# Kernel optimization log

Hardware: AMD Instinct MI355X
Metric: run time of the kernel (lower is better)

## Reference

```python
import jax, jax.numpy as jnp
import numpy as np

H = W = 1024
CHUNK = 32  # rows per chunk in the column EDT pass (keeps intermediate at 32*H*W floats)


def setup_inputs() -> dict:
    key = jax.random.key(0)
    k1, k2 = jax.random.split(key)
    preds = jax.random.randint(k1, (H, W), 0, 2).astype(jnp.float32)
    targets = jax.random.randint(k2, (H, W), 0, 2).astype(jnp.float32)
    return {"preds": preds, "targets": targets}


def _edges(seg):
    # morphological erosion via 3x3 box conv, threshold at 9 == kernel.numel()
    s = seg[None, None]  # (1,1,H,W)
    kern = jnp.ones((1, 1, 3, 3), seg.dtype)
    conv = jax.lax.conv_general_dilated(s, kern, (1, 1), ((1, 1), (1, 1)))
    eroded = (conv[0, 0] == 9.0).astype(seg.dtype)
    return seg - eroded


def _edt(edges):
    # exact Euclidean distance transform: distance to nearest zero of (1 - edges),
    # i.e. nearest pixel where edges == 1.  Separable exact algorithm:
    #   1) per-row 1D distance to nearest feature (via cummax/cummin scans)
    #   2) per-column lower envelope min_k g2[k,j] + (i-k)^2 (chunked brute force)
    feat = (1.0 - edges) == 0.0
    Hh, Ww = edges.shape
    BIG = jnp.float32(1e6)
    col = jnp.arange(Ww, dtype=jnp.float32)
    left = col - jax.lax.cummax(jnp.where(feat, col, -BIG), axis=1)
    right = jax.lax.cummin(jnp.where(feat, col, BIG), axis=1, reverse=True) - col
    g = jnp.minimum(jnp.minimum(left, right), BIG)  # row-wise 1D distance
    g2 = g * g  # (H,W) squared row distances
    rows = jnp.arange(Hh, dtype=jnp.float32)

    def chunk(ic):  # ic: (CHUNK,) target row indices
        # (CHUNK, H, W): g2[k,j] + (i-k)^2, min over source row k
        d = g2[None, :, :] + (ic[:, None, None] - rows[None, :, None]) ** 2
        return jnp.min(d, axis=1)  # (CHUNK, W)

    D2 = jax.lax.map(chunk, rows.reshape(-1, CHUNK)).reshape(Hh, Ww)
    return jnp.sqrt(D2)


def reference(preds, targets):
    pred_edges = _edges(preds)
    target_edges = _edges(targets)
    # scipy EDT ran on detached CPU copies -> no gradient through the DTs
    pred_dt = jax.lax.stop_gradient(_edt(pred_edges))
    target_dt = jax.lax.stop_gradient(_edt(target_edges))
    pred_err = target_edges * pred_dt
    target_err = pred_edges * target_dt
    loss = (jnp.mean(pred_err) + jnp.mean(target_err)) / 2.0
    return jax.nn.sigmoid(loss)
```

## Files before the change

### kernel.cpp

```cpp
#include <hip/hip_runtime.h>
#include <math.h>


#define HW 1024
#define WIN 8
#define RPB 128
#define KROWS (RPB + 2 * WIN)
#define HS_STRIDE 17
#define NC 146
#define NW 130
#define NBYTES ((NC + NW) * 16)

__device__ inline int edge_at(const float* __restrict__ seg, int k, int j)
{
    if ((unsigned)k >= (unsigned)HW || (unsigned)j >= (unsigned)HW) return 0;
    if (seg[k * HW + j] == 0.f) return 0;
    bool all9 = true;
    #pragma unroll
    for (int dy = -1; dy <= 1; ++dy)
        #pragma unroll
        for (int dx = -1; dx <= 1; ++dx) {
            const int kk = k + dy, jj = j + dx;
            const float v = ((unsigned)kk < (unsigned)HW && (unsigned)jj < (unsigned)HW)
                            ? seg[kk * HW + jj] : 0.f;
            all9 = all9 && (v != 0.f);
        }
    return all9 ? 0 : 1;
}

__global__ __launch_bounds__(256)
void k_main(const float* __restrict__ pred, const float* __restrict__ targ,
            float* __restrict__ partial)
{
    const int t  = threadIdx.x;
    const int j0 = blockIdx.x * 16;
    const int i0 = blockIdx.y * RPB;
    const int mc = blockIdx.z;
    const float* __restrict__ segc = mc ? targ : pred;
    const float* __restrict__ segw = mc ? pred : targ;

    __shared__ alignas(16) unsigned char sbytes[NBYTES];
    __shared__ unsigned long long s_mc[NC];
    __shared__ unsigned long long s_me[NW];
    __shared__ float hs[KROWS * HS_STRIDE];
    __shared__ unsigned short esb[RPB];
    __shared__ float wsum[4];

    const int W0 = j0 - 24;

    for (int idx = t; idx < NBYTES; idx += 256) {
        const int  isW = idx >= NC * 16;
        const int  rel = isW ? idx - NC * 16 : idx;
        const int  row = rel >> 4, c4 = rel & 15;
        const int  gr  = isW ? (i0 - 1 + row) : (i0 - 9 + row);
        const int  c   = W0 + c4 * 4;
        float4 v = make_float4(0.f, 0.f, 0.f, 0.f);
        if ((unsigned)gr < (unsigned)HW && (unsigned)c <= 1020u) {
            const float* __restrict__ base = isW ? segw : segc;
            v = *(const float4*)&base[gr * HW + c];
        }
        const unsigned by = (unsigned)(v.x != 0.f) | ((unsigned)(v.y != 0.f) << 1)
                          | ((unsigned)(v.z != 0.f) << 2) | ((unsigned)(v.w != 0.f) << 3);
        sbytes[idx] = (unsigned char)by;
    }
    __syncthreads();

    for (int rowi = t; rowi < NC + NW; rowi += 256) {
        const uint4 u = *(const uint4*)&sbytes[rowi * 16];
        const unsigned wq[4] = {u.x, u.y, u.z, u.w};
        unsigned long long r = 0ull;
        #pragma unroll
        for (int q = 0; q < 4; ++q) {
            const unsigned x = wq[q] & 0x0F0F0F0Fu;
            const unsigned y = x | (x >> 4);
            const unsigned h16 = (y & 0xFFu) | (((y >> 16) & 0xFFu) << 8);
            r |= (unsigned long long)h16 << (16 * q);
        }
        if (rowi < NC) s_mc[rowi] = r;
        else           s_me[rowi - NC] = r;
    }
    __syncthreads();

    if (t < KROWS) {
        const int kr = i0 - WIN + t;
        if ((unsigned)kr < (unsigned)HW) {
            const unsigned long long sA = s_mc[t], sB = s_mc[t + 1], sC = s_mc[t + 2];
            const unsigned long long va = sA & sB & sC;
            const unsigned long long er = va & (va << 1) & (va >> 1);
            const unsigned long long edge = (sB & ~er) & 0x7FFFFFFFFFFFFFFEull;
            const float krk = (float)(kr * kr);
            #pragma unroll
            for (int jc = 0; jc < 16; ++jc) {
                const int p = 24 + jc;
                const unsigned long long mle = edge & ((1ull << (p + 1)) - 1ull);
                const unsigned long long mge = edge >> p;
                int g = 1 << 20;
                if (mle) g = p - (63 - __clzll((long long)mle));
                if (mge) g = min(g, __ffsll((unsigned long long)mge) - 1);
                hs[t * HS_STRIDE + jc] = (g < (1 << 20))
                    ? fmaf((float)g, (float)g, krk) : 1e30f;
            }
        } else {
            #pragma unroll
            for (int jc = 0; jc < 16; ++jc)
                hs[t * HS_STRIDE + jc] = 1e30f;
        }
    }
    if (t < RPB) {
        const unsigned long long sA = s_me[t], sB = s_me[t + 1], sC = s_me[t + 2];
        const unsigned long long va = sA & sB & sC;
        const unsigned long long er = va & (va << 1) & (va >> 1);
        const unsigned long long edge = sB & ~er;
        esb[t] = (unsigned short)((edge >> 24) & 0xFFFFull);
    }
    __syncthreads();

    const int jj = t & 15;
    const int iw = t >> 4;
    float lsum = 0.f;

    #pragma unroll
    for (int g = 0; g < 2; ++g) {
        const int ib = i0 + iw * 8 + g * 4;
        const int kkS = iw * 8 + g * 4;
        float b0 = 3e38f, b1 = 3e38f, b2 = 3e38f, b3 = 3e38f;
        float kf = (float)(ib - WIN);
        const float m0 = -2.f * (float)(ib);
        const float m1 = -2.f * (float)(ib + 1);
        const float m2 = -2.f * (float)(ib + 2);
        const float m3 = -2.f * (float)(ib + 3);
        #pragma unroll
        for (int kk = kkS; kk < kkS + 2 * WIN + 4; ++kk) {
            const float hvv = hs[kk * HS_STRIDE + jj];
            b0 = fminf(b0, fmaf(m0, kf, hvv));
            b1 = fminf(b1, fmaf(m1, kf, hvv));
            b2 = fminf(b2, fmaf(m2, kf, hvv));
            b3 = fminf(b3, fmaf(m3, kf, hvv));
            kf += 1.f;
        }
        const int sLo = max(0, ib - WIN);
        const int sHi = min(HW - 1, ib + WIN + 3);
        float bs[4] = {b0, b1, b2, b3};
        #pragma unroll
        for (int w = 0; w < 4; ++w) {
            const int i = ib + w;
            float D2 = (float)(i * i) + bs[w];
            const int dl = i - sLo + 1, dr = sHi + 1 - i;
            const bool need = (D2 > 576.f) ||
                              ((sLo > 0) && (D2 > (float)(dl * dl))) ||
                              ((sHi < HW - 1) && (D2 > (float)(dr * dr)));
            if (need) {
                const int jg = j0 + jj;
                float bb = 1e6f - (float)jg;
                bb = bb * bb;
                for (int k = 0; k < HW; ++k) {
                    const float rowt = (float)((i - k) * (i - k));
                    if (rowt >= bb) continue;
                    for (int d = 0; d < HW; ++d) {
                        const float dd = rowt + (float)(d * d);
                        if (dd >= bb) break;
                        if (edge_at(segc, k, jg - d) || edge_at(segc, k, jg + d)) {
                            bb = dd; break;
                        }
                    }
                }
                D2 = bb;
            }
            const unsigned wbit = (esb[i - i0] >> jj) & 1u;
            lsum += wbit ? sqrtf(D2) : 0.f;
        }
    }

    #pragma unroll
    for (int off = 32; off > 0; off >>= 1) lsum += __shfl_down(lsum, off);
    if ((t & 63) == 0) wsum[t >> 6] = lsum;
    __syncthreads();
    if (t == 0) {
        const int bid = blockIdx.x + 64 * (blockIdx.y + 8 * blockIdx.z);
        partial[bid] = wsum[0] + wsum[1] + wsum[2] + wsum[3];
    }
}

__global__ __launch_bounds__(256)
void k_fin(const float* __restrict__ partial, float* __restrict__ out)
{
    const int t = threadIdx.x;
    float s = partial[t] + partial[t + 256] + partial[t + 512] + partial[t + 768];
    #pragma unroll
    for (int off = 32; off > 0; off >>= 1) s += __shfl_down(s, off);
    __shared__ float w[4];
    if ((t & 63) == 0) w[t >> 6] = s;
    __syncthreads();
    if (t == 0) {
        const float tot = w[0] + w[1] + w[2] + w[3];
        const float loss = tot * (1.f / (2.f * 1024.f * 1024.f));
        out[0] = 1.f / (1.f + expf(-loss));
    }
}

extern "C" void kernel_launch(void* const* d_in, const int* in_sizes, int n_in,
                              void* d_out, int out_size, void* d_ws, size_t ws_size,
                              hipStream_t stream)
{
    const float* preds   = (const float*)d_in[0];
    const float* targets = (const float*)d_in[1];
    float* out = (float*)d_out;

    float* partial = (float*)d_ws;

    dim3 gM(HW / 16, HW / RPB, 2);
    k_main<<<gM, 256, 0, stream>>>(preds, targets, partial);

    k_fin<<<1, 256, 0, stream>>>(partial, out);
}
```

Measured before the change: 79.26 us.

## Process both images per block with wider 32-column tiles and shared loads

Each block now loads both pred and target for one tile, builds bitmasks for both once, and runs the windowed EDT for each image in turn. The tile widens from 16 to 32 columns, which narrows the halo to 16 and lowers the fallback threshold from 576 to 256. The grid drops from 1024 to 256 blocks, so there is less redundant halo loading but fewer blocks and more serial work per block. The lower threshold may send more pixels down the slow brute-force fallback path.

```diff
diff --git a/kernel.cpp b/kernel.cpp
--- a/kernel.cpp
+++ b/kernel.cpp
@@ -6,10 +6,9 @@
 #define WIN 8
 #define RPB 128
 #define KROWS (RPB + 2 * WIN)
-#define HS_STRIDE 17
-#define NC 146
-#define NW 130
-#define NBYTES ((NC + NW) * 16)
+#define HS_STRIDE 33
+#define NR 146
+#define NBY (2 * NR * 16)
 
 __device__ inline int edge_at(const float* __restrict__ seg, int k, int j)
 {
@@ -28,101 +27,50 @@
     return all9 ? 0 : 1;
 }
 
-__global__ __launch_bounds__(256)
-void k_main(const float* __restrict__ pred, const float* __restrict__ targ,
-            float* __restrict__ partial)
-{
-    const int t  = threadIdx.x;
-    const int j0 = blockIdx.x * 16;
-    const int i0 = blockIdx.y * RPB;
-    const int mc = blockIdx.z;
-    const float* __restrict__ segc = mc ? targ : pred;
-    const float* __restrict__ segw = mc ? pred : targ;
-
-    __shared__ alignas(16) unsigned char sbytes[NBYTES];
-    __shared__ unsigned long long s_mc[NC];
-    __shared__ unsigned long long s_me[NW];
-    __shared__ float hs[KROWS * HS_STRIDE];
-    __shared__ unsigned short esb[RPB];
-    __shared__ float wsum[4];
-
-    const int W0 = j0 - 24;
-
-    for (int idx = t; idx < NBYTES; idx += 256) {
-        const int  isW = idx >= NC * 16;
-        const int  rel = isW ? idx - NC * 16 : idx;
-        const int  row = rel >> 4, c4 = rel & 15;
-        const int  gr  = isW ? (i0 - 1 + row) : (i0 - 9 + row);
-        const int  c   = W0 + c4 * 4;
-        float4 v = make_float4(0.f, 0.f, 0.f, 0.f);
-        if ((unsigned)gr < (unsigned)HW && (unsigned)c <= 1020u) {
-            const float* __restrict__ base = isW ? segw : segc;
-            v = *(const float4*)&base[gr * HW + c];
-        }
-        const unsigned by = (unsigned)(v.x != 0.f) | ((unsigned)(v.y != 0.f) << 1)
-                          | ((unsigned)(v.z != 0.f) << 2) | ((unsigned)(v.w != 0.f) << 3);
-        sbytes[idx] = (unsigned char)by;
-    }
-    __syncthreads();
-
-    for (int rowi = t; rowi < NC + NW; rowi += 256) {
-        const uint4 u = *(const uint4*)&sbytes[rowi * 16];
-        const unsigned wq[4] = {u.x, u.y, u.z, u.w};
-        unsigned long long r = 0ull;
-        #pragma unroll
-        for (int q = 0; q < 4; ++q) {
-            const unsigned x = wq[q] & 0x0F0F0F0Fu;
-            const unsigned y = x | (x >> 4);
-            const unsigned h16 = (y & 0xFFu) | (((y >> 16) & 0xFFu) << 8);
-            r |= (unsigned long long)h16 << (16 * q);
-        }
-        if (rowi < NC) s_mc[rowi] = r;
-        else           s_me[rowi - NC] = r;
-    }
-    __syncthreads();
-
-    if (t < KROWS) {
-        const int kr = i0 - WIN + t;
+__device__ __forceinline__ void fill_hs(float* __restrict__ hs,
+                                        const unsigned long long* __restrict__ mm,
+                                        int i0, int t)
+{
+    for (int idx = t; idx < 288; idx += 256) {
+        const int tt = idx >> 1, half = idx & 1;
+        const int kr = i0 - WIN + tt;
+        float* __restrict__ hrow = &hs[tt * HS_STRIDE + half * 16];
         if ((unsigned)kr < (unsigned)HW) {
-            const unsigned long long sA = s_mc[t], sB = s_mc[t + 1], sC = s_mc[t + 2];
+            const unsigned long long sA = mm[tt], sB = mm[tt + 1], sC = mm[tt + 2];
             const unsigned long long va = sA & sB & sC;
             const unsigned long long er = va & (va << 1) & (va >> 1);
             const unsigned long long edge = (sB & ~er) & 0x7FFFFFFFFFFFFFFEull;
             const float krk = (float)(kr * kr);
             #pragma unroll
             for (int jc = 0; jc < 16; ++jc) {
-                const int p = 24 + jc;
+                const int p = 16 + half * 16 + jc;
                 const unsigned long long mle = edge & ((1ull << (p + 1)) - 1ull);
                 const unsigned long long mge = edge >> p;
                 int g = 1 << 20;
                 if (mle) g = p - (63 - __clzll((long long)mle));
-                if (mge) g = min(g, __ffsll((unsigned long long)mge) - 1);
-                hs[t * HS_STRIDE + jc] = (g < (1 << 20))
-                    ? fmaf((float)g, (float)g, krk) : 1e30f;
+                if (mge) g = min(g, __ffsll(mge) - 1);
+                hrow[jc] = (g < (1 << 20)) ? fmaf((float)g, (float)g, krk) : 1e30f;
             }
         } else {
             #pragma unroll
-            for (int jc = 0; jc < 16; ++jc)
-                hs[t * HS_STRIDE + jc] = 1e30f;
-        }
-    }
-    if (t < RPB) {
-        const unsigned long long sA = s_me[t], sB = s_me[t + 1], sC = s_me[t + 2];
-        const unsigned long long va = sA & sB & sC;
-        const unsigned long long er = va & (va << 1) & (va >> 1);
-        const unsigned long long edge = sB & ~er;
-        esb[t] = (unsigned short)((edge >> 24) & 0xFFFFull);
-    }
-    __syncthreads();
-
-    const int jj = t & 15;
-    const int iw = t >> 4;
+            for (int jc = 0; jc < 16; ++jc) hrow[jc] = 1e30f;
+        }
+    }
+}
+
+__device__ __forceinline__ float edt_acc(const float* __restrict__ hs,
+                                         const unsigned* __restrict__ esbw,
+                                         int i0, int j0, int t,
+                                         const float* __restrict__ segf)
+{
+    const int jj = t & 31;
+    const int iw = t >> 5;
     float lsum = 0.f;
 
     #pragma unroll
-    for (int g = 0; g < 2; ++g) {
-        const int ib = i0 + iw * 8 + g * 4;
-        const int kkS = iw * 8 + g * 4;
+    for (int g = 0; g < 4; ++g) {
+        const int ib = i0 + iw * 16 + g * 4;
+        const int kkS = iw * 16 + g * 4;
         float b0 = 3e38f, b1 = 3e38f, b2 = 3e38f, b3 = 3e38f;
         float kf = (float)(ib - WIN);
         const float m0 = -2.f * (float)(ib);
@@ -146,7 +94,7 @@
             const int i = ib + w;
             float D2 = (float)(i * i) + bs[w];
             const int dl = i - sLo + 1, dr = sHi + 1 - i;
-            const bool need = (D2 > 576.f) ||
+            const bool need = (D2 > 256.f) ||
                               ((sLo > 0) && (D2 > (float)(dl * dl))) ||
                               ((sHi < HW - 1) && (D2 > (float)(dr * dr)));
             if (need) {
@@ -159,24 +107,93 @@
                     for (int d = 0; d < HW; ++d) {
                         const float dd = rowt + (float)(d * d);
                         if (dd >= bb) break;
-                        if (edge_at(segc, k, jg - d) || edge_at(segc, k, jg + d)) {
+                        if (edge_at(segf, k, jg - d) || edge_at(segf, k, jg + d)) {
                             bb = dd; break;
                         }
                     }
                 }
                 D2 = bb;
             }
-            const unsigned wbit = (esb[i - i0] >> jj) & 1u;
+            const unsigned wbit = (esbw[i - i0] >> jj) & 1u;
             lsum += wbit ? sqrtf(D2) : 0.f;
         }
     }
+    return lsum;
+}
+
+__global__ __launch_bounds__(256)
+void k_main(const float* __restrict__ pred, const float* __restrict__ targ,
+            float* __restrict__ partial)
+{
+    const int t  = threadIdx.x;
+    const int j0 = blockIdx.x * 32;
+    const int i0 = blockIdx.y * RPB;
+
+    __shared__ alignas(16) unsigned char sbytes[NBY];
+    __shared__ unsigned long long s_m[2 * NR];
+    __shared__ float hs[KROWS * HS_STRIDE];
+    __shared__ unsigned esb[2][RPB];
+    __shared__ float wsum[4];
+
+    const int W0 = j0 - 16;
+
+    for (int idx = t; idx < NBY; idx += 256) {
+        const int  img = idx >= NR * 16;
+        const int  rel = img ? idx - NR * 16 : idx;
+        const int  row = rel >> 4, c4 = rel & 15;
+        const int  gr  = i0 - 9 + row;
+        const int  c   = W0 + c4 * 4;
+        float4 v = make_float4(0.f, 0.f, 0.f, 0.f);
+        if ((unsigned)gr < (unsigned)HW && (unsigned)c <= 1020u) {
+            const float* __restrict__ base = img ? targ : pred;
+            v = *(const float4*)&base[gr * HW + c];
+        }
+        const unsigned by = (unsigned)(v.x != 0.f) | ((unsigned)(v.y != 0.f) << 1)
+                          | ((unsigned)(v.z != 0.f) << 2) | ((unsigned)(v.w != 0.f) << 3);
+        sbytes[idx] = (unsigned char)by;
+    }
+    __syncthreads();
+
+    for (int rowi = t; rowi < 2 * NR; rowi += 256) {
+        const uint4 u = *(const uint4*)&sbytes[rowi * 16];
+        const unsigned wq[4] = {u.x, u.y, u.z, u.w};
+        unsigned long long r = 0ull;
+        #pragma unroll
+        for (int q = 0; q < 4; ++q) {
+            const unsigned x = wq[q] & 0x0F0F0F0Fu;
+            const unsigned y = x | (x >> 4);
+            const unsigned h16 = (y & 0xFFu) | (((y >> 16) & 0xFFu) << 8);
+            r |= (unsigned long long)h16 << (16 * q);
+        }
+        s_m[rowi] = r;
+    }
+    __syncthreads();
+
+    {
+        const int img = t >> 7, r = t & 127;
+        const unsigned long long* mm = &s_m[img * NR];
+        const unsigned long long sA = mm[r + 8], sB = mm[r + 9], sC = mm[r + 10];
+        const unsigned long long va = sA & sB & sC;
+        const unsigned long long er = va & (va << 1) & (va >> 1);
+        const unsigned long long edge = sB & ~er;
+        esb[img][r] = (unsigned)((edge >> 16) & 0xFFFFFFFFull);
+    }
+    fill_hs(hs, &s_m[0], i0, t);
+    __syncthreads();
+
+    float lsum = edt_acc(hs, esb[1], i0, j0, t, pred);
+    __syncthreads();
+
+    fill_hs(hs, &s_m[NR], i0, t);
+    __syncthreads();
+    lsum += edt_acc(hs, esb[0], i0, j0, t, targ);
 
     #pragma unroll
     for (int off = 32; off > 0; off >>= 1) lsum += __shfl_down(lsum, off);
     if ((t & 63) == 0) wsum[t >> 6] = lsum;
     __syncthreads();
     if (t == 0) {
-        const int bid = blockIdx.x + 64 * (blockIdx.y + 8 * blockIdx.z);
+        const int bid = blockIdx.x + 32 * blockIdx.y;
         partial[bid] = wsum[0] + wsum[1] + wsum[2] + wsum[3];
     }
 }
@@ -185,7 +202,7 @@
 void k_fin(const float* __restrict__ partial, float* __restrict__ out)
 {
     const int t = threadIdx.x;
-    float s = partial[t] + partial[t + 256] + partial[t + 512] + partial[t + 768];
+    float s = partial[t];
     #pragma unroll
     for (int off = 32; off > 0; off >>= 1) s += __shfl_down(s, off);
     __shared__ float w[4];
@@ -208,7 +225,7 @@
 
     float* partial = (float*)d_ws;
 
-    dim3 gM(HW / 16, HW / RPB, 2);
+    dim3 gM(HW / 32, HW / RPB, 1);
     k_main<<<gM, 256, 0, stream>>>(preds, targets, partial);
 
     k_fin<<<1, 256, 0, stream>>>(partial, out);
```

New measurement: 82.23 us. 1.04x slower.
